# Performance work log

Hardware: AMD Instinct MI355X
Metric: run time of the kernel (lower is better)

Reference implementation:

```python
import jax, jax.numpy as jnp
import numpy as np

N, E, B = 50000, 400000, 128
F_IN, EDIM, EMB, H = 64, 8, 64, 4
HC = EMB * H  # 256
L = 3          # gnn_layers
DN = 256       # dense_neurons
NEG_SLOPE = 0.2
EPS = 1e-5


def setup_inputs():
    key = jax.random.key(0)
    ks = jax.random.split(key, 32)
    s = 0.05
    d = {}
    d["x"] = jax.random.normal(ks[0], (N, F_IN), jnp.float32)
    d["edge_index"] = jax.random.randint(ks[1], (2, E), 0, N, jnp.int32)
    d["edge_attr"] = jax.random.normal(ks[2], (E, EDIM), jnp.float32)
    d["mol_formal_charge"] = jax.random.normal(ks[3], (B,), jnp.float32)
    d["mol_nrot"] = jax.random.normal(ks[4], (B,), jnp.float32)
    d["batch_index"] = jnp.sort(jax.random.randint(ks[5], (N,), 0, B, jnp.int32))
    # GATv2 params, stacked over L layers (in_dim == EMB == F_IN for all layers)
    d["gat_Wl"] = jax.random.normal(ks[6], (L, F_IN, HC), jnp.float32) * s
    d["gat_Wr"] = jax.random.normal(ks[7], (L, F_IN, HC), jnp.float32) * s
    d["gat_We"] = jax.random.normal(ks[8], (L, EDIM, HC), jnp.float32) * s
    d["gat_att"] = jax.random.normal(ks[9], (L, H, EMB), jnp.float32) * s
    d["gat_b"] = jnp.zeros((L, HC), jnp.float32)
    d["tr_W"] = jax.random.normal(ks[10], (L, HC, EMB), jnp.float32) * s
    d["tr_b"] = jnp.zeros((L, EMB), jnp.float32)
    d["bn_g"] = jnp.ones((L, EMB), jnp.float32)
    d["bn_b"] = jnp.zeros((L, EMB), jnp.float32)
    d["gate_W"] = jax.random.normal(ks[11], (EMB, 1), jnp.float32) * s
    d["gate_b"] = jnp.zeros((1,), jnp.float32)
    d["lin1_W"] = jax.random.normal(ks[12], (EMB + 2, DN), jnp.float32) * s
    d["lin1_b"] = jnp.zeros((DN,), jnp.float32)
    d["fc1_W"] = jax.random.normal(ks[13], (DN, DN // 2), jnp.float32) * s
    d["fc1_b"] = jnp.zeros((DN // 2,), jnp.float32)
    d["fc2_W"] = jax.random.normal(ks[14], (DN // 2, DN // 4), jnp.float32) * s
    d["fc2_b"] = jnp.zeros((DN // 4,), jnp.float32)
    d["out_W"] = jax.random.normal(ks[15], (DN // 4, 1), jnp.float32) * s
    d["out_b"] = jnp.zeros((1,), jnp.float32)
    return d


def _seg_softmax(logits, seg, num):
    # numerically stable per-segment softmax over leading axis
    mx = jax.ops.segment_max(logits, seg, num_segments=num)
    ex = jnp.exp(logits - mx[seg])
    den = jax.ops.segment_sum(ex, seg, num_segments=num)
    return ex / den[seg]


def reference(x, edge_index, edge_attr, mol_formal_charge, mol_nrot, batch_index,
              gat_Wl, gat_Wr, gat_We, gat_att, gat_b, tr_W, tr_b, bn_g, bn_b,
              gate_W, gate_b, lin1_W, lin1_b, fc1_W, fc1_b, fc2_W, fc2_b,
              out_W, out_b):
    src, dst = edge_index[0], edge_index[1]  # messages flow src -> dst
    h = x
    for l in range(L):
        xl = (h @ gat_Wl[l]).reshape(N, H, EMB)
        xr = (h @ gat_Wr[l]).reshape(N, H, EMB)
        ea = (edge_attr @ gat_We[l]).reshape(E, H, EMB)
        xls = xl[src]                                   # [E,H,C]
        m = jax.nn.leaky_relu(xls + xr[dst] + ea, NEG_SLOPE)
        logit = jnp.einsum('ehc,hc->eh', m, gat_att[l])  # [E,H]
        alpha = _seg_softmax(logit, dst, N)              # [E,H]
        agg = jax.ops.segment_sum(alpha[:, :, None] * xls, dst, num_segments=N)
        h = agg.reshape(N, HC) + gat_b[l]
        h = jax.nn.relu(h @ tr_W[l] + tr_b[l])
        # BatchNorm1d (training-mode batch stats, biased var)
        mu = h.mean(0)
        var = h.var(0)
        h = (h - mu) / jnp.sqrt(var + EPS) * bn_g[l] + bn_b[l]
    # AttentionalAggregation pooling
    gate = h @ gate_W + gate_b                           # [N,1]
    w = _seg_softmax(gate, batch_index, B)
    pooled = jax.ops.segment_sum(w * h, batch_index, num_segments=B)  # [B,EMB]
    z = jnp.concatenate([pooled, mol_formal_charge[:, None], mol_nrot[:, None]], axis=1)
    z = jax.nn.relu(z @ lin1_W + lin1_b)
    z = jax.nn.relu(z @ fc1_W + fc1_b)
    z = jax.nn.relu(z @ fc2_W + fc2_b)
    return z @ out_W + out_b                             # [B,1]
```

## Files before the change

kernel.cpp:

```cpp
#include <hip/hip_runtime.h>

#define NN 50000
#define NE 400000
#define NB 128
#define NINF (-__builtin_inff())

__device__ __forceinline__ float dpp_add16(float x) {
    int v = __float_as_int(x);
    x += __int_as_float(__builtin_amdgcn_update_dpp(0, v, 0xB1, 0xF, 0xF, true));
    v = __float_as_int(x);
    x += __int_as_float(__builtin_amdgcn_update_dpp(0, v, 0x4E, 0xF, 0xF, true));
    v = __float_as_int(x);
    x += __int_as_float(__builtin_amdgcn_update_dpp(0, v, 0x141, 0xF, 0xF, true));
    v = __float_as_int(x);
    x += __int_as_float(__builtin_amdgcn_update_dpp(0, v, 0x140, 0xF, 0xF, true));
    return x;
}

__global__ __launch_bounds__(256) void k_hist(const int* __restrict__ dstv, int* __restrict__ deg) {
    int e = blockIdx.x * 256 + threadIdx.x;
    if (e < NE) atomicAdd(&deg[dstv[e]], 1);
}

__global__ __launch_bounds__(256) void k_scan1(const int* __restrict__ deg, int* __restrict__ bsum) {
    __shared__ int ws[4];
    const int tid = threadIdx.x, lane = tid & 63, w = tid >> 6;
    const int i = blockIdx.x * 256 + tid;
    int v = (i < NN) ? deg[i] : 0;
    #pragma unroll
    for (int off = 32; off; off >>= 1) v += __shfl_xor(v, off);
    if (lane == 0) ws[w] = v;
    __syncthreads();
    if (tid == 0) bsum[blockIdx.x] = ws[0] + ws[1] + ws[2] + ws[3];
}

__global__ __launch_bounds__(256) void k_scan2(const int* __restrict__ bsum, int* __restrict__ boff, int nblk) {
    __shared__ int ws[4];
    const int tid = threadIdx.x, lane = tid & 63, w = tid >> 6;
    int v = (tid < nblk) ? bsum[tid] : 0;
    int incl = v;
    #pragma unroll
    for (int off = 1; off < 64; off <<= 1) {
        int t = __shfl_up(incl, off);
        if (lane >= off) incl += t;
    }
    if (lane == 63) ws[w] = incl;
    __syncthreads();
    int add = 0;
    for (int k = 0; k < w; ++k) add += ws[k];
    if (tid < nblk) boff[tid] = add + incl - v;
}

__global__ __launch_bounds__(256) void k_scan3(const int* __restrict__ deg, const int* __restrict__ boff,
                                               int* __restrict__ rowptr) {
    __shared__ int ws[4];
    const int tid = threadIdx.x, lane = tid & 63, w = tid >> 6;
    const int i = blockIdx.x * 256 + tid;
    int v = (i < NN) ? deg[i] : 0;
    int incl = v;
    #pragma unroll
    for (int off = 1; off < 64; off <<= 1) {
        int t = __shfl_up(incl, off);
        if (lane >= off) incl += t;
    }
    if (lane == 63) ws[w] = incl;
    __syncthreads();
    int add = boff[blockIdx.x];
    for (int k = 0; k < w; ++k) add += ws[k];
    if (i < NN) rowptr[i + 1] = add + incl;
    if (i == 0) rowptr[0] = 0;
}

__global__ __launch_bounds__(256) void k_scatter(const int* __restrict__ dstv, const int* __restrict__ srcv,
                                                 const float* __restrict__ eattr, const int* __restrict__ rowptr,
                                                 int* __restrict__ cnt, int* __restrict__ eid,
                                                 int* __restrict__ src_perm, float4* __restrict__ ea_perm,
                                                 int use_perm) {
    int e = blockIdx.x * 256 + threadIdx.x;
    if (e < NE) {
        int d = dstv[e];
        int pos = rowptr[d] + atomicAdd(&cnt[d], 1);
        eid[pos] = e;
        if (use_perm) {
            src_perm[pos] = srcv[e];
            ea_perm[(size_t)pos * 2] = ((const float4*)eattr)[e * 2];
            ea_perm[(size_t)pos * 2 + 1] = ((const float4*)eattr)[e * 2 + 1];
        }
    }
}

__global__ __launch_bounds__(256) void k_gemm64(const float* __restrict__ A, const float* __restrict__ Wl,
                                                const float* __restrict__ Wr, float* __restrict__ Cl,
                                                float* __restrict__ Cr, const float* __restrict__ stats,
                                                const float* __restrict__ bg, const float* __restrict__ bb) {
    __shared__ float At[64 * 132];
    __shared__ float Ws[64 * 128];
    __shared__ float sc_s[64], sh_s[64], shW_s[128];
    const int tid = threadIdx.x;
    const int mat = blockIdx.y >> 1, ch = blockIdx.y & 1;
    const float* W = mat ? Wr : Wl;
    float* C = mat ? Cr : Cl;
    const int r0b = blockIdx.x * 128;

    if (stats) {
        if (tid < 64) {
            const float mu = stats[tid] * (1.0f / (float)NN);
            const float var = stats[64 + tid] * (1.0f / (float)NN) - mu * mu;
            const float rstd = rsqrtf(var + 1e-5f);
            const float sc = bg[tid] * rstd;
            sc_s[tid] = sc;
            sh_s[tid] = fmaf(-mu, sc, bb[tid]);
        }
        __syncthreads();
    }
    for (int i = tid; i < 2048; i += 256) {
        const int k = i >> 5, c4 = i & 31;
        float4 v = ((const float4*)W)[k * 64 + ch * 32 + c4];
        if (stats) {
            const float s = sc_s[k];
            v.x *= s; v.y *= s; v.z *= s; v.w *= s;
        }
        ((float4*)Ws)[i] = v;
    }
    for (int i = tid; i < 2048; i += 256) {
        const int r = i >> 4, kq = i & 15;
        const int rg = (r0b + r < NN) ? (r0b + r) : (NN - 1);
        const float4 v = ((const float4*)A)[rg * 16 + kq];
        At[(kq * 4 + 0) * 132 + r] = v.x;
        At[(kq * 4 + 1) * 132 + r] = v.y;
        At[(kq * 4 + 2) * 132 + r] = v.z;
        At[(kq * 4 + 3) * 132 + r] = v.w;
    }
    if (stats && tid < 128) {
        const float* wc = W + ch * 128 + tid;
        float s = 0.f;
        for (int k = 0; k < 64; ++k) s = fmaf(sh_s[k], wc[k * 256], s);
        shW_s[tid] = s;
    }
    __syncthreads();

    const int cg = tid & 15;
    const int rg = tid >> 4;
    float acc[8][8];
    if (stats) {
        #pragma unroll
        for (int rr = 0; rr < 8; ++rr)
            #pragma unroll
            for (int j = 0; j < 8; ++j)
                acc[rr][j] = (j < 4) ? shW_s[cg * 4 + j] : shW_s[64 + cg * 4 + (j - 4)];
    } else {
        #pragma unroll
        for (int rr = 0; rr < 8; ++rr)
            #pragma unroll
            for (int j = 0; j < 8; ++j) acc[rr][j] = 0.f;
    }

    #pragma unroll 4
    for (int k = 0; k < 64; ++k) {
        const float4 a0 = *(const float4*)(At + k * 132 + rg * 8);
        const float4 a1 = *(const float4*)(At + k * 132 + rg * 8 + 4);
        const float4 w0 = *(const float4*)(Ws + k * 128 + cg * 4);
        const float4 w1 = *(const float4*)(Ws + k * 128 + 64 + cg * 4);
        const float ar[8] = {a0.x, a0.y, a0.z, a0.w, a1.x, a1.y, a1.z, a1.w};
        #pragma unroll
        for (int rr = 0; rr < 8; ++rr) {
            acc[rr][0] = fmaf(ar[rr], w0.x, acc[rr][0]);
            acc[rr][1] = fmaf(ar[rr], w0.y, acc[rr][1]);
            acc[rr][2] = fmaf(ar[rr], w0.z, acc[rr][2]);
            acc[rr][3] = fmaf(ar[rr], w0.w, acc[rr][3]);
            acc[rr][4] = fmaf(ar[rr], w1.x, acc[rr][4]);
            acc[rr][5] = fmaf(ar[rr], w1.y, acc[rr][5]);
            acc[rr][6] = fmaf(ar[rr], w1.z, acc[rr][6]);
            acc[rr][7] = fmaf(ar[rr], w1.w, acc[rr][7]);
        }
    }
    #pragma unroll
    for (int rr = 0; rr < 8; ++rr) {
        const int r = r0b + rg * 8 + rr;
        if (r < NN) {
            float* cp = C + (size_t)r * 256 + ch * 128 + cg * 4;
            *(float4*)cp = make_float4(acc[rr][0], acc[rr][1], acc[rr][2], acc[rr][3]);
            *(float4*)(cp + 64) = make_float4(acc[rr][4], acc[rr][5], acc[rr][6], acc[rr][7]);
        }
    }
}

template <bool PERM>
__global__ __launch_bounds__(256, 4) void k_agg(const float* __restrict__ xl, float* __restrict__ xragg,
                                                const float* __restrict__ att, const float* __restrict__ gatb,
                                                const int* __restrict__ rowptr, const int* __restrict__ eid,
                                                const int* __restrict__ srcv, const float* __restrict__ eattr,
                                                const int* __restrict__ src_perm, const float4* __restrict__ ea_perm,
                                                const float* __restrict__ We) {
    const int lane = threadIdx.x & 63;
    const float4 we0 = ((const float4*)(We + 0 * 256))[lane];
    const float4 we1 = ((const float4*)(We + 1 * 256))[lane];
    const float4 we2 = ((const float4*)(We + 2 * 256))[lane];
    const float4 we3 = ((const float4*)(We + 3 * 256))[lane];
    const float4 we4 = ((const float4*)(We + 4 * 256))[lane];
    const float4 we5 = ((const float4*)(We + 5 * 256))[lane];
    const float4 we6 = ((const float4*)(We + 6 * 256))[lane];
    const float4 we7 = ((const float4*)(We + 7 * 256))[lane];
    const float4 attf = ((const float4*)att)[lane];
    const float4 gbf = ((const float4*)gatb)[lane];
    const int nw = gridDim.x * (blockDim.x >> 6);
    int wid = blockIdx.x * (blockDim.x >> 6) + (threadIdx.x >> 6);

#define LOADE(X, idx)                                                          \
    {                                                                          \
        int s_;                                                                \
        const float4* eap_;                                                    \
        if (PERM) {                                                            \
            s_ = src_perm[idx];                                                \
            eap_ = ea_perm + (size_t)(idx) * 2;                                \
        } else {                                                               \
            const int e_ = eid[idx];                                           \
            s_ = srcv[e_];                                                     \
            eap_ = (const float4*)(eattr + (size_t)e_ * 8);                    \
        }                                                                      \
        X##x = ((const float4*)(xl + (size_t)s_ * 256))[lane];                 \
        X##a = eap_[0];                                                        \
        X##b = eap_[1];                                                        \
    }

#define PROC(X)                                                                \
    {                                                                          \
        float v0 = fmaf(X##a.x, we0.x, xr.x), v1 = fmaf(X##a.x, we0.y, xr.y);  \
        float v2 = fmaf(X##a.x, we0.z, xr.z), v3 = fmaf(X##a.x, we0.w, xr.w);  \
        v0 = fmaf(X##a.y, we1.x, v0); v1 = fmaf(X##a.y, we1.y, v1);            \
        v2 = fmaf(X##a.y, we1.z, v2); v3 = fmaf(X##a.y, we1.w, v3);            \
        v0 = fmaf(X##a.z, we2.x, v0); v1 = fmaf(X##a.z, we2.y, v1);            \
        v2 = fmaf(X##a.z, we2.z, v2); v3 = fmaf(X##a.z, we2.w, v3);            \
        v0 = fmaf(X##a.w, we3.x, v0); v1 = fmaf(X##a.w, we3.y, v1);            \
        v2 = fmaf(X##a.w, we3.z, v2); v3 = fmaf(X##a.w, we3.w, v3);            \
        v0 = fmaf(X##b.x, we4.x, v0); v1 = fmaf(X##b.x, we4.y, v1);            \
        v2 = fmaf(X##b.x, we4.z, v2); v3 = fmaf(X##b.x, we4.w, v3);            \
        v0 = fmaf(X##b.y, we5.x, v0); v1 = fmaf(X##b.y, we5.y, v1);            \
        v2 = fmaf(X##b.y, we5.z, v2); v3 = fmaf(X##b.y, we5.w, v3);            \
        v0 = fmaf(X##b.z, we6.x, v0); v1 = fmaf(X##b.z, we6.y, v1);            \
        v2 = fmaf(X##b.z, we6.z, v2); v3 = fmaf(X##b.z, we6.w, v3);            \
        v0 = fmaf(X##b.w, we7.x, v0); v1 = fmaf(X##b.w, we7.y, v1);            \
        v2 = fmaf(X##b.w, we7.z, v2); v3 = fmaf(X##b.w, we7.w, v3);            \
        v0 += X##x.x; v1 += X##x.y; v2 += X##x.z; v3 += X##x.w;                \
        v0 = fmaxf(v0, 0.2f * v0); v1 = fmaxf(v1, 0.2f * v1);                  \
        v2 = fmaxf(v2, 0.2f * v2); v3 = fmaxf(v3, 0.2f * v3);                  \
        float part = v0 * attf.x;                                              \
        part = fmaf(v1, attf.y, part);                                         \
        part = fmaf(v2, attf.z, part);                                         \
        part = fmaf(v3, attf.w, part);                                         \
        part = dpp_add16(part);                                                \
        const float p = __expf(part);                                          \
        den += p;                                                              \
        c0 = fmaf(p, X##x.x, c0);                                              \
        c1 = fmaf(p, X##x.y, c1);                                              \
        c2 = fmaf(p, X##x.z, c2);                                              \
        c3 = fmaf(p, X##x.w, c3);                                              \
    }

    for (int n = wid; n < NN; n += nw) {
        const int e0 = rowptr[n], e1 = rowptr[n + 1];
        const float4 xr = ((const float4*)(xragg + (size_t)n * 256))[lane];
        float den = 0.f, c0 = 0.f, c1 = 0.f, c2 = 0.f, c3 = 0.f;
        float4 Ax, Aa, Ab, Bx, Ba, Bb;
        const int cnt = e1 - e0;
        if (cnt > 0) {
            LOADE(A, e0);
            if (cnt > 1) {
                LOADE(B, e0 + 1);
                int i = e0;
                for (; i + 3 < e1; i += 2) {
                    PROC(A);
                    LOADE(A, i + 2);
                    PROC(B);
                    LOADE(B, i + 3);
                }
                const int r = e1 - i;
                PROC(A);
                if (r == 3) {
                    LOADE(A, i + 2);
                    PROC(B);
                    PROC(A);
                } else {
                    PROC(B);
                }
            } else {
                PROC(A);
            }
        }
        float4 o;
        if (cnt > 0) {
            const float inv = 1.0f / den;
            o.x = fmaf(c0, inv, gbf.x);
            o.y = fmaf(c1, inv, gbf.y);
            o.z = fmaf(c2, inv, gbf.z);
            o.w = fmaf(c3, inv, gbf.w);
        } else {
            o = gbf;
        }
        ((float4*)(xragg + (size_t)n * 256))[lane] = o;
    }
#undef LOADE
#undef PROC
}

__global__ __launch_bounds__(128) void k_tr(const float* __restrict__ A, const float* __restrict__ W,
                                            const float* __restrict__ bias, float* __restrict__ Hout,
                                            float* __restrict__ stats) {
    __shared__ float At[32 * 132];
    __shared__ float Ws[32 * 64];
    __shared__ float red[128];
    const int tid = threadIdx.x;
    const int cg = tid & 7;
    const int rg = tid >> 3;
    const int r0b = blockIdx.x * 128;

    float acc[8][8];
    #pragma unroll
    for (int rr = 0; rr < 8; ++rr)
        #pragma unroll
        for (int j = 0; j < 8; ++j)
            acc[rr][j] = bias[(j < 4) ? (cg * 4 + j) : (32 + cg * 4 + (j - 4))];

    for (int kc = 0; kc < 8; ++kc) {
        if (kc) __syncthreads();
        for (int i = tid; i < 512; i += 128)
            ((float4*)Ws)[i] = ((const float4*)(W + kc * 2048))[i];
        for (int i = tid; i < 1024; i += 128) {
            const int r = i >> 3, c4 = i & 7;
            const int rgl = (r0b + r < NN) ? (r0b + r) : (NN - 1);
            const float4 v = ((const float4*)A)[(size_t)rgl * 64 + kc * 8 + c4];
            At[(c4 * 4 + 0) * 132 + r] = v.x;
            At[(c4 * 4 + 1) * 132 + r] = v.y;
            At[(c4 * 4 + 2) * 132 + r] = v.z;
            At[(c4 * 4 + 3) * 132 + r] = v.w;
        }
        __syncthreads();
        #pragma unroll 4
        for (int k = 0; k < 32; ++k) {
            const float4 a0 = *(const float4*)(At + k * 132 + rg * 8);
            const float4 a1 = *(const float4*)(At + k * 132 + rg * 8 + 4);
            const float4 w0 = *(const float4*)(Ws + k * 64 + cg * 4);
            const float4 w1 = *(const float4*)(Ws + k * 64 + 32 + cg * 4);
            const float ar[8] = {a0.x, a0.y, a0.z, a0.w, a1.x, a1.y, a1.z, a1.w};
            #pragma unroll
            for (int rr = 0; rr < 8; ++rr) {
                acc[rr][0] = fmaf(ar[rr], w0.x, acc[rr][0]);
                acc[rr][1] = fmaf(ar[rr], w0.y, acc[rr][1]);
                acc[rr][2] = fmaf(ar[rr], w0.z, acc[rr][2]);
                acc[rr][3] = fmaf(ar[rr], w0.w, acc[rr][3]);
                acc[rr][4] = fmaf(ar[rr], w1.x, acc[rr][4]);
                acc[rr][5] = fmaf(ar[rr], w1.y, acc[rr][5]);
                acc[rr][6] = fmaf(ar[rr], w1.z, acc[rr][6]);
                acc[rr][7] = fmaf(ar[rr], w1.w, acc[rr][7]);
            }
        }
    }
    float lsum[8], lsq[8];
    #pragma unroll
    for (int j = 0; j < 8; ++j) { lsum[j] = 0.f; lsq[j] = 0.f; }
    #pragma unroll
    for (int rr = 0; rr < 8; ++rr) {
        const int r = r0b + rg * 8 + rr;
        if (r < NN) {
            float v[8];
            #pragma unroll
            for (int j = 0; j < 8; ++j) {
                v[j] = fmaxf(acc[rr][j], 0.f);
                lsum[j] += v[j];
                lsq[j] = fmaf(v[j], v[j], lsq[j]);
            }
            float* hp = Hout + (size_t)r * 64;
            *(float4*)(hp + cg * 4) = make_float4(v[0], v[1], v[2], v[3]);
            *(float4*)(hp + 32 + cg * 4) = make_float4(v[4], v[5], v[6], v[7]);
        }
    }
    __syncthreads();
    red[tid] = 0.f;
    __syncthreads();
    #pragma unroll
    for (int j = 0; j < 8; ++j) {
        const int c = (j < 4) ? (cg * 4 + j) : (32 + cg * 4 + (j - 4));
        atomicAdd(&red[c], lsum[j]);
        atomicAdd(&red[64 + c], lsq[j]);
    }
    __syncthreads();
    if (tid < 64) {
        atomicAdd(&stats[tid], red[tid]);
        atomicAdd(&stats[64 + tid], red[64 + tid]);
    }
}

__global__ __launch_bounds__(256) void k_poolhead(const float* __restrict__ h, const float* __restrict__ gw,
                                                  const int* __restrict__ bidx, const float* __restrict__ stats,
                                                  const float* __restrict__ bg, const float* __restrict__ bb,
                                                  const float* __restrict__ fc, const float* __restrict__ nrot,
                                                  const float* __restrict__ W1, const float* __restrict__ b1,
                                                  const float* __restrict__ W2, const float* __restrict__ b2,
                                                  const float* __restrict__ W3, const float* __restrict__ b3,
                                                  const float* __restrict__ W4, const float* __restrict__ b4,
                                                  float* __restrict__ out) {
    __shared__ float gate_s[1024];
    __shared__ float red[4];
    __shared__ float pp[4][64];
    __shared__ float scb[64], shb[64];
    __shared__ float z[66], a1[256], a2[128], a3[64];
    const int b = blockIdx.x, tid = threadIdx.x, lane = tid & 63, w = tid >> 6;
    if (tid < 64) {
        const float mu = stats[tid] * (1.0f / (float)NN);
        const float var = stats[64 + tid] * (1.0f / (float)NN) - mu * mu;
        const float rstd = rsqrtf(var + 1e-5f);
        const float sc = bg[tid] * rstd;
        scb[tid] = sc;
        shb[tid] = fmaf(-mu, sc, bb[tid]);
    }
    int lo = 0, hi = NN;
    while (lo < hi) { int mid = (lo + hi) >> 1; if (bidx[mid] < b) lo = mid + 1; else hi = mid; }
    const int s0 = lo;
    lo = 0; hi = NN;
    while (lo < hi) { int mid = (lo + hi) >> 1; if (bidx[mid] < b + 1) lo = mid + 1; else hi = mid; }
    const int s1 = lo;
    const int seg = s1 - s0;
    __syncthreads();

    const float gwv = gw[lane] * scb[lane];
    for (int i = s0 + w; i < s1; i += 4) {
        float p = h[(size_t)i * 64 + lane] * gwv;
        #pragma unroll
        for (int off = 32; off; off >>= 1) p += __shfl_xor(p, off);
        if (lane == 0) gate_s[i - s0] = p;
    }
    __syncthreads();
    float v = NINF;
    for (int i = tid; i < seg; i += 256) v = fmaxf(v, gate_s[i]);
    #pragma unroll
    for (int off = 32; off; off >>= 1) v = fmaxf(v, __shfl_xor(v, off));
    if (lane == 0) red[w] = v;
    __syncthreads();
    const float mx = fmaxf(fmaxf(red[0], red[1]), fmaxf(red[2], red[3]));
    __syncthreads();
    float d = 0.f;
    for (int i = tid; i < seg; i += 256) {
        const float ex = __expf(gate_s[i] - mx);
        gate_s[i] = ex;
        d += ex;
    }
    #pragma unroll
    for (int off = 32; off; off >>= 1) d += __shfl_xor(d, off);
    if (lane == 0) red[w] = d;
    __syncthreads();
    const float den = red[0] + red[1] + red[2] + red[3];
    const int c = tid & 63, ro = tid >> 6;
    float acc = 0.f;
    for (int i = s0 + ro; i < s1; i += 4) acc = fmaf(gate_s[i - s0], h[(size_t)i * 64 + c], acc);
    pp[ro][c] = acc;
    __syncthreads();
    if (tid < 64) {
        const float raw = (pp[0][tid] + pp[1][tid] + pp[2][tid] + pp[3][tid]) / den;
        z[tid] = (seg > 0) ? fmaf(raw, scb[tid], shb[tid]) : shb[tid];
    }
    if (tid == 64) z[64] = fc[b];
    if (tid == 65) z[65] = nrot[b];
    __syncthreads();
    float s = b1[tid];
    for (int k = 0; k < 66; ++k) s = fmaf(z[k], W1[k * 256 + tid], s);
    a1[tid] = fmaxf(s, 0.f);
    __syncthreads();
    if (tid < 128) {
        float s2 = b2[tid];
        for (int k = 0; k < 256; ++k) s2 = fmaf(a1[k], W2[k * 128 + tid], s2);
        a2[tid] = fmaxf(s2, 0.f);
    }
    __syncthreads();
    if (tid < 64) {
        float s3 = b3[tid];
        for (int k = 0; k < 128; ++k) s3 = fmaf(a2[k], W3[k * 64 + tid], s3);
        a3[tid] = fmaxf(s3, 0.f);
    }
    __syncthreads();
    if (tid < 64) {
        float p = a3[tid] * W4[tid];
        #pragma unroll
        for (int off = 32; off; off >>= 1) p += __shfl_xor(p, off);
        if (tid == 0) out[b] = p + b4[0];
    }
}

extern "C" void kernel_launch(void* const* d_in, const int* in_sizes, int n_in,
                              void* d_out, int out_size, void* d_ws, size_t ws_size,
                              hipStream_t stream) {
    const float* x     = (const float*)d_in[0];
    const int*   ei    = (const int*)d_in[1];
    const float* eattr = (const float*)d_in[2];
    const float* fcv   = (const float*)d_in[3];
    const float* nrot  = (const float*)d_in[4];
    const int*   bidx  = (const int*)d_in[5];
    const float* Wl    = (const float*)d_in[6];
    const float* Wr    = (const float*)d_in[7];
    const float* We    = (const float*)d_in[8];
    const float* att   = (const float*)d_in[9];
    const float* gatb  = (const float*)d_in[10];
    const float* trW   = (const float*)d_in[11];
    const float* trb   = (const float*)d_in[12];
    const float* bng   = (const float*)d_in[13];
    const float* bnb   = (const float*)d_in[14];
    const float* gateW = (const float*)d_in[15];
    const float* W1    = (const float*)d_in[17];
    const float* b1    = (const float*)d_in[18];
    const float* W2    = (const float*)d_in[19];
    const float* b2    = (const float*)d_in[20];
    const float* W3    = (const float*)d_in[21];
    const float* b3    = (const float*)d_in[22];
    const float* W4    = (const float*)d_in[23];
    const float* b4    = (const float*)d_in[24];
    float* out = (float*)d_out;

    const int* srcv = ei;
    const int* dstv = ei + NE;

    char* w = (char*)d_ws;
    float*  xl       = (float*)(w);
    float*  xragg    = (float*)(w + 51200000);
    float*  hbuf     = (float*)(w + 102400000);
    int*    deg      = (int*)  (w + 102400000);
    int*    cnt      = (int*)  (w + 102600000);
    int*    eid      = (int*)  (w + 115200000);
    int*    rowptr   = (int*)  (w + 116800000);
    float*  stats    = (float*)(w + 117000064);
    int*    bsum     = (int*)  (w + 117004096);
    int*    boff     = (int*)  (w + 117006144);
    int*    src_perm = (int*)  (w + 117042048);
    float4* ea_perm  = (float4*)(w + 118642048);
    const bool use_perm = (ws_size >= (size_t)131442048);
    const int NBLK = (NN + 255) / 256;

    hipMemsetAsync(deg, 0, 400000, stream);
    hipMemsetAsync(stats, 0, 1536, stream);
    k_hist<<<(NE + 255) / 256, 256, 0, stream>>>(dstv, deg);
    k_scan1<<<NBLK, 256, 0, stream>>>(deg, bsum);
    k_scan2<<<1, 256, 0, stream>>>(bsum, boff, NBLK);
    k_scan3<<<NBLK, 256, 0, stream>>>(deg, boff, rowptr);
    k_scatter<<<(NE + 255) / 256, 256, 0, stream>>>(dstv, srcv, eattr, rowptr, cnt, eid,
                                                    src_perm, ea_perm, use_perm ? 1 : 0);

    const float* hin = x;
    for (int l = 0; l < 3; ++l) {
        const float* st = (l == 0) ? nullptr : (stats + (l - 1) * 128);
        const float* g  = (l == 0) ? nullptr : (bng + (l - 1) * 64);
        const float* bb = (l == 0) ? nullptr : (bnb + (l - 1) * 64);
        dim3 gg((NN + 127) / 128, 4);
        k_gemm64<<<gg, 256, 0, stream>>>(hin, Wl + l * 16384, Wr + l * 16384, xl, xragg, st, g, bb);
        if (use_perm)
            k_agg<true><<<2048, 256, 0, stream>>>(xl, xragg, att + l * 256, gatb + l * 256, rowptr,
                                                  eid, srcv, eattr, src_perm, ea_perm, We + l * 2048);
        else
            k_agg<false><<<2048, 256, 0, stream>>>(xl, xragg, att + l * 256, gatb + l * 256, rowptr,
                                                   eid, srcv, eattr, src_perm, ea_perm, We + l * 2048);
        k_tr<<<(NN + 127) / 128, 128, 0, stream>>>(xragg, trW + l * 16384, trb + l * 64, hbuf, stats + l * 128);
        hin = hbuf;
    }
    k_poolhead<<<NB, 256, 0, stream>>>(hbuf, gateW, bidx, stats + 2 * 128, bng + 128, bnb + 128,
                                       fcv, nrot, W1, b1, W2, b2, W3, b3, W4, b4, out);
}
```

Measured before the change: 754.7 us.

## Split gemm K into chunks, triple-buffer agg edge loads, widen k_tr tiles

The node GEMM now stages its operands in two K-chunks of 32, which halves its shared-memory footprint, and declares launch bounds of 4 blocks per SM to raise occupancy. The aggregation loop now keeps three edges' loads in flight instead of two, to hide more gather latency at the cost of extra registers. The transform GEMM moves to 256-thread blocks covering 256 rows, with each thread's output columns made contiguous, which changes the stats reduction layout. Together these aim to cut latency and occupancy limits across the per-layer kernels.

After: 698.6 us. 1.08x faster.

```diff
diff --git a/kernel.cpp b/kernel.cpp
--- a/kernel.cpp
+++ b/kernel.cpp
@@ -89,18 +89,20 @@
     }
 }
 
-__global__ __launch_bounds__(256) void k_gemm64(const float* __restrict__ A, const float* __restrict__ Wl,
-                                                const float* __restrict__ Wr, float* __restrict__ Cl,
-                                                float* __restrict__ Cr, const float* __restrict__ stats,
-                                                const float* __restrict__ bg, const float* __restrict__ bb) {
-    __shared__ float At[64 * 132];
-    __shared__ float Ws[64 * 128];
+__global__ __launch_bounds__(256, 4) void k_gemm64(const float* __restrict__ A, const float* __restrict__ Wl,
+                                                   const float* __restrict__ Wr, float* __restrict__ Cl,
+                                                   float* __restrict__ Cr, const float* __restrict__ stats,
+                                                   const float* __restrict__ bg, const float* __restrict__ bb) {
+    __shared__ float At[32 * 132];
+    __shared__ float Ws[32 * 128];
     __shared__ float sc_s[64], sh_s[64], shW_s[128];
     const int tid = threadIdx.x;
     const int mat = blockIdx.y >> 1, ch = blockIdx.y & 1;
     const float* W = mat ? Wr : Wl;
     float* C = mat ? Cr : Cl;
     const int r0b = blockIdx.x * 128;
+    const int cg = tid & 15;
+    const int rg = tid >> 4;
 
     if (stats) {
         if (tid < 64) {
@@ -112,35 +114,15 @@
             sh_s[tid] = fmaf(-mu, sc, bb[tid]);
         }
         __syncthreads();
-    }
-    for (int i = tid; i < 2048; i += 256) {
-        const int k = i >> 5, c4 = i & 31;
-        float4 v = ((const float4*)W)[k * 64 + ch * 32 + c4];
-        if (stats) {
-            const float s = sc_s[k];
-            v.x *= s; v.y *= s; v.z *= s; v.w *= s;
-        }
-        ((float4*)Ws)[i] = v;
-    }
-    for (int i = tid; i < 2048; i += 256) {
-        const int r = i >> 4, kq = i & 15;
-        const int rg = (r0b + r < NN) ? (r0b + r) : (NN - 1);
-        const float4 v = ((const float4*)A)[rg * 16 + kq];
-        At[(kq * 4 + 0) * 132 + r] = v.x;
-        At[(kq * 4 + 1) * 132 + r] = v.y;
-        At[(kq * 4 + 2) * 132 + r] = v.z;
-        At[(kq * 4 + 3) * 132 + r] = v.w;
-    }
-    if (stats && tid < 128) {
-        const float* wc = W + ch * 128 + tid;
-        float s = 0.f;
-        for (int k = 0; k < 64; ++k) s = fmaf(sh_s[k], wc[k * 256], s);
-        shW_s[tid] = s;
-    }
-    __syncthreads();
-
-    const int cg = tid & 15;
-    const int rg = tid >> 4;
+        if (tid < 128) {
+            const float* wc = W + ch * 128 + tid;
+            float s = 0.f;
+            for (int k = 0; k < 64; ++k) s = fmaf(sh_s[k], wc[k * 256], s);
+            shW_s[tid] = s;
+        }
+        __syncthreads();
+    }
+
     float acc[8][8];
     if (stats) {
         #pragma unroll
@@ -155,23 +137,45 @@
             for (int j = 0; j < 8; ++j) acc[rr][j] = 0.f;
     }
 
-    #pragma unroll 4
-    for (int k = 0; k < 64; ++k) {
-        const float4 a0 = *(const float4*)(At + k * 132 + rg * 8);
-        const float4 a1 = *(const float4*)(At + k * 132 + rg * 8 + 4);
-        const float4 w0 = *(const float4*)(Ws + k * 128 + cg * 4);
-        const float4 w1 = *(const float4*)(Ws + k * 128 + 64 + cg * 4);
-        const float ar[8] = {a0.x, a0.y, a0.z, a0.w, a1.x, a1.y, a1.z, a1.w};
-        #pragma unroll
-        for (int rr = 0; rr < 8; ++rr) {
-            acc[rr][0] = fmaf(ar[rr], w0.x, acc[rr][0]);
-            acc[rr][1] = fmaf(ar[rr], w0.y, acc[rr][1]);
-            acc[rr][2] = fmaf(ar[rr], w0.z, acc[rr][2]);
-            acc[rr][3] = fmaf(ar[rr], w0.w, acc[rr][3]);
-            acc[rr][4] = fmaf(ar[rr], w1.x, acc[rr][4]);
-            acc[rr][5] = fmaf(ar[rr], w1.y, acc[rr][5]);
-            acc[rr][6] = fmaf(ar[rr], w1.z, acc[rr][6]);
-            acc[rr][7] = fmaf(ar[rr], w1.w, acc[rr][7]);
+    for (int kc = 0; kc < 2; ++kc) {
+        if (kc) __syncthreads();
+        for (int i = tid; i < 1024; i += 256) {
+            const int k = i >> 5, c4 = i & 31;
+            float4 v = ((const float4*)W)[(kc * 32 + k) * 64 + ch * 32 + c4];
+            if (stats) {
+                const float s = sc_s[kc * 32 + k];
+                v.x *= s; v.y *= s; v.z *= s; v.w *= s;
+            }
+            ((float4*)Ws)[i] = v;
+        }
+        for (int i = tid; i < 1024; i += 256) {
+            const int r = i >> 3, c4 = i & 7;
+            const int rgl = (r0b + r < NN) ? (r0b + r) : (NN - 1);
+            const float4 v = ((const float4*)A)[rgl * 16 + kc * 8 + c4];
+            At[(c4 * 4 + 0) * 132 + r] = v.x;
+            At[(c4 * 4 + 1) * 132 + r] = v.y;
+            At[(c4 * 4 + 2) * 132 + r] = v.z;
+            At[(c4 * 4 + 3) * 132 + r] = v.w;
+        }
+        __syncthreads();
+        #pragma unroll 4
+        for (int k = 0; k < 32; ++k) {
+            const float4 a0 = *(const float4*)(At + k * 132 + rg * 8);
+            const float4 a1 = *(const float4*)(At + k * 132 + rg * 8 + 4);
+            const float4 w0 = *(const float4*)(Ws + k * 128 + cg * 4);
+            const float4 w1 = *(const float4*)(Ws + k * 128 + 64 + cg * 4);
+            const float ar[8] = {a0.x, a0.y, a0.z, a0.w, a1.x, a1.y, a1.z, a1.w};
+            #pragma unroll
+            for (int rr = 0; rr < 8; ++rr) {
+                acc[rr][0] = fmaf(ar[rr], w0.x, acc[rr][0]);
+                acc[rr][1] = fmaf(ar[rr], w0.y, acc[rr][1]);
+                acc[rr][2] = fmaf(ar[rr], w0.z, acc[rr][2]);
+                acc[rr][3] = fmaf(ar[rr], w0.w, acc[rr][3]);
+                acc[rr][4] = fmaf(ar[rr], w1.x, acc[rr][4]);
+                acc[rr][5] = fmaf(ar[rr], w1.y, acc[rr][5]);
+                acc[rr][6] = fmaf(ar[rr], w1.z, acc[rr][6]);
+                acc[rr][7] = fmaf(ar[rr], w1.w, acc[rr][7]);
+            }
         }
     }
     #pragma unroll
@@ -261,31 +265,27 @@
         const int e0 = rowptr[n], e1 = rowptr[n + 1];
         const float4 xr = ((const float4*)(xragg + (size_t)n * 256))[lane];
         float den = 0.f, c0 = 0.f, c1 = 0.f, c2 = 0.f, c3 = 0.f;
-        float4 Ax, Aa, Ab, Bx, Ba, Bb;
+        float4 Ax, Aa, Ab, Bx, Ba, Bb, Cx, Ca, Cb;
         const int cnt = e1 - e0;
         if (cnt > 0) {
             LOADE(A, e0);
-            if (cnt > 1) {
-                LOADE(B, e0 + 1);
-                int i = e0;
-                for (; i + 3 < e1; i += 2) {
-                    PROC(A);
-                    LOADE(A, i + 2);
-                    PROC(B);
-                    LOADE(B, i + 3);
-                }
-                const int r = e1 - i;
+            if (cnt > 1) LOADE(B, e0 + 1);
+            if (cnt > 2) LOADE(C, e0 + 2);
+            int i = e0;
+            for (; i + 5 < e1; i += 3) {
                 PROC(A);
-                if (r == 3) {
-                    LOADE(A, i + 2);
-                    PROC(B);
-                    PROC(A);
-                } else {
-                    PROC(B);
-                }
-            } else {
-                PROC(A);
+                LOADE(A, i + 3);
+                PROC(B);
+                LOADE(B, i + 4);
+                PROC(C);
+                LOADE(C, i + 5);
             }
+            const int m = e1 - i;
+            PROC(A);
+            if (m >= 2) PROC(B);
+            if (m >= 3) PROC(C);
+            if (m >= 4) { LOADE(A, i + 3); PROC(A); }
+            if (m == 5) { LOADE(B, i + 4); PROC(B); }
         }
         float4 o;
         if (cnt > 0) {
@@ -303,44 +303,44 @@
 #undef PROC
 }
 
-__global__ __launch_bounds__(128) void k_tr(const float* __restrict__ A, const float* __restrict__ W,
-                                            const float* __restrict__ bias, float* __restrict__ Hout,
-                                            float* __restrict__ stats) {
-    __shared__ float At[32 * 132];
+__global__ __launch_bounds__(256, 4) void k_tr(const float* __restrict__ A, const float* __restrict__ W,
+                                               const float* __restrict__ bias, float* __restrict__ Hout,
+                                               float* __restrict__ stats) {
+    __shared__ float At[32 * 260];
     __shared__ float Ws[32 * 64];
     __shared__ float red[128];
     const int tid = threadIdx.x;
     const int cg = tid & 7;
     const int rg = tid >> 3;
-    const int r0b = blockIdx.x * 128;
+    const int r0b = blockIdx.x * 256;
 
     float acc[8][8];
     #pragma unroll
     for (int rr = 0; rr < 8; ++rr)
         #pragma unroll
         for (int j = 0; j < 8; ++j)
-            acc[rr][j] = bias[(j < 4) ? (cg * 4 + j) : (32 + cg * 4 + (j - 4))];
+            acc[rr][j] = bias[cg * 8 + j];
 
     for (int kc = 0; kc < 8; ++kc) {
         if (kc) __syncthreads();
-        for (int i = tid; i < 512; i += 128)
+        for (int i = tid; i < 512; i += 256)
             ((float4*)Ws)[i] = ((const float4*)(W + kc * 2048))[i];
-        for (int i = tid; i < 1024; i += 128) {
+        for (int i = tid; i < 2048; i += 256) {
             const int r = i >> 3, c4 = i & 7;
             const int rgl = (r0b + r < NN) ? (r0b + r) : (NN - 1);
             const float4 v = ((const float4*)A)[(size_t)rgl * 64 + kc * 8 + c4];
-            At[(c4 * 4 + 0) * 132 + r] = v.x;
-            At[(c4 * 4 + 1) * 132 + r] = v.y;
-            At[(c4 * 4 + 2) * 132 + r] = v.z;
-            At[(c4 * 4 + 3) * 132 + r] = v.w;
+            At[(c4 * 4 + 0) * 260 + r] = v.x;
+            At[(c4 * 4 + 1) * 260 + r] = v.y;
+            At[(c4 * 4 + 2) * 260 + r] = v.z;
+            At[(c4 * 4 + 3) * 260 + r] = v.w;
         }
         __syncthreads();
         #pragma unroll 4
         for (int k = 0; k < 32; ++k) {
-            const float4 a0 = *(const float4*)(At + k * 132 + rg * 8);
-            const float4 a1 = *(const float4*)(At + k * 132 + rg * 8 + 4);
-            const float4 w0 = *(const float4*)(Ws + k * 64 + cg * 4);
-            const float4 w1 = *(const float4*)(Ws + k * 64 + 32 + cg * 4);
+            const float4 a0 = *(const float4*)(At + k * 260 + rg * 8);
+            const float4 a1 = *(const float4*)(At + k * 260 + rg * 8 + 4);
+            const float4 w0 = *(const float4*)(Ws + k * 64 + cg * 8);
+            const float4 w1 = *(const float4*)(Ws + k * 64 + cg * 8 + 4);
             const float ar[8] = {a0.x, a0.y, a0.z, a0.w, a1.x, a1.y, a1.z, a1.w};
             #pragma unroll
             for (int rr = 0; rr < 8; ++rr) {
@@ -370,18 +370,17 @@
                 lsq[j] = fmaf(v[j], v[j], lsq[j]);
             }
             float* hp = Hout + (size_t)r * 64;
-            *(float4*)(hp + cg * 4) = make_float4(v[0], v[1], v[2], v[3]);
-            *(float4*)(hp + 32 + cg * 4) = make_float4(v[4], v[5], v[6], v[7]);
-        }
-    }
-    __syncthreads();
-    red[tid] = 0.f;
+            *(float4*)(hp + cg * 8) = make_float4(v[0], v[1], v[2], v[3]);
+            *(float4*)(hp + cg * 8 + 4) = make_float4(v[4], v[5], v[6], v[7]);
+        }
+    }
+    __syncthreads();
+    if (tid < 128) red[tid] = 0.f;
     __syncthreads();
     #pragma unroll
     for (int j = 0; j < 8; ++j) {
-        const int c = (j < 4) ? (cg * 4 + j) : (32 + cg * 4 + (j - 4));
-        atomicAdd(&red[c], lsum[j]);
-        atomicAdd(&red[64 + c], lsq[j]);
+        atomicAdd(&red[cg * 8 + j], lsum[j]);
+        atomicAdd(&red[64 + cg * 8 + j], lsq[j]);
     }
     __syncthreads();
     if (tid < 64) {
@@ -555,7 +554,7 @@
         else
             k_agg<false><<<2048, 256, 0, stream>>>(xl, xragg, att + l * 256, gatb + l * 256, rowptr,
                                                    eid, srcv, eattr, src_perm, ea_perm, We + l * 2048);
-        k_tr<<<(NN + 127) / 128, 128, 0, stream>>>(xragg, trW + l * 16384, trb + l * 64, hbuf, stats + l * 128);
+        k_tr<<<(NN + 255) / 256, 256, 0, stream>>>(xragg, trW + l * 16384, trb + l * 64, hbuf, stats + l * 128);
         hin = hbuf;
     }
     k_poolhead<<<NB, 256, 0, stream>>>(hbuf, gateW, bidx, stats + 2 * 128, bng + 128, bnb + 128,
```
